# Optimization experiments

Measured on AMD Instinct MI355X. Metric: run time of the kernel, lower is better.

The kernel has to match this reference:

```python
import jax, jax.numpy as jnp
import numpy as np

BN_EPS = 1e-5
NUM_GRAPHS = 64

def _bn(h, gamma, beta):
    # BatchNorm1d over node dim, training-mode (batch statistics, biased var)
    mu = jnp.mean(h, axis=0)
    var = jnp.mean(jnp.square(h - mu), axis=0)
    return gamma * (h - mu) * jax.lax.rsqrt(var + BN_EPS) + beta

def _gin_conv(x, src, dst, Wa, ba, gamma, beta, Wb, bb):
    # sum-aggregate neighbor features: agg[v] = sum_{(u,v) in E} x[u]
    n = x.shape[0]
    agg = jax.ops.segment_sum(x[src], dst, num_segments=n)
    h = x + agg  # eps = 0 (default GINConv)
    h = jax.nn.relu(_bn(h @ Wa + ba, gamma, beta))
    return jax.nn.relu(h @ Wb + bb)

def setup_inputs() -> dict:
    key = jax.random.key(0)
    ks = jax.random.split(key, 16)
    N, E, IN, D, OUT = 50000, 800000, 128, 512, 10
    x = jax.random.normal(ks[0], (N, IN), dtype=jnp.float32)
    edge_index = jax.random.randint(ks[1], (2, E), 0, N, dtype=jnp.int64)
    batch = jnp.sort(jax.random.randint(ks[2], (N,), 0, NUM_GRAPHS, dtype=jnp.int64))
    def lin(k, i, o):
        return jax.random.normal(k, (i, o), dtype=jnp.float32) / np.sqrt(i)
    return {
        "x": x, "edge_index": edge_index, "batch": batch,
        "W1a": lin(ks[3], IN, D), "b1a": jnp.zeros((D,), jnp.float32),
        "g1": jnp.ones((D,), jnp.float32), "be1": jnp.zeros((D,), jnp.float32),
        "W1b": lin(ks[4], D, D), "b1b": jnp.zeros((D,), jnp.float32),
        "W2a": lin(ks[5], D, D), "b2a": jnp.zeros((D,), jnp.float32),
        "g2": jnp.ones((D,), jnp.float32), "be2": jnp.zeros((D,), jnp.float32),
        "W2b": lin(ks[6], D, D), "b2b": jnp.zeros((D,), jnp.float32),
        "Wl1": lin(ks[7], D, D), "bl1": jnp.zeros((D,), jnp.float32),
        "Wl2": lin(ks[8], D, OUT), "bl2": jnp.zeros((OUT,), jnp.float32),
    }

def reference(x, edge_index, batch, W1a, b1a, g1, be1, W1b, b1b,
              W2a, b2a, g2, be2, W2b, b2b, Wl1, bl1, Wl2, bl2):
    src, dst = edge_index[0], edge_index[1]
    h = _gin_conv(x, src, dst, W1a, b1a, g1, be1, W1b, b1b)
    h = _gin_conv(h, src, dst, W2a, b2a, g2, be2, W2b, b2b)
    pooled = jax.ops.segment_sum(h, batch, num_segments=NUM_GRAPHS)  # [G, D]
    out = jax.nn.relu(pooled @ Wl1 + bl1)
    return out @ Wl2 + bl2  # [G, out_channels]
```

## Files before the change

kernel.cpp:

```cpp
#include <hip/hip_runtime.h>
#include <cstdint>
#include <cstddef>

#define N_NODES  50000
#define N_EDGES  800000
#define DIM_IN   128
#define DIM_H    512
#define N_GRAPHS 64
#define DIM_OUT  10
#define BN_EPS   1e-5f
#define SCAN_B   196

typedef _Float16 h16;
using f16x8 = __attribute__((ext_vector_type(8))) _Float16;
using f32x4 = __attribute__((ext_vector_type(4))) float;

__device__ inline float4 add4(float4 a, float4 b) {
    return make_float4(a.x + b.x, a.y + b.y, a.z + b.z, a.w + b.w);
}

__global__ __launch_bounds__(256) void k_wcast_all(
    const float* __restrict__ W1a, const float* __restrict__ W1b,
    const float* __restrict__ W2a, const float* __restrict__ W2b,
    h16* __restrict__ Wt1a, h16* __restrict__ Wt1b,
    h16* __restrict__ Wt2a, h16* __restrict__ Wt2b,
    int* __restrict__ deg, float* __restrict__ pooled)
{
    int gtid = blockIdx.x * 256 + threadIdx.x;
    for (int i = gtid; i < N_NODES; i += 416 * 256) deg[i] = 0;
    for (int i = gtid; i < N_GRAPHS * DIM_H; i += 416 * 256) pooled[i] = 0.f;

    int b = blockIdx.x;
    const float* W; h16* Wt; int K, base;
    if (b < 32)       { W = W1a; Wt = Wt1a; K = DIM_IN; base = 0; }
    else if (b < 160) { W = W1b; Wt = Wt1b; K = DIM_H;  base = 32; }
    else if (b < 288) { W = W2a; Wt = Wt2a; K = DIM_H;  base = 160; }
    else              { W = W2b; Wt = Wt2b; K = DIM_H;  base = 288; }
    int t = (b - base) * 256 + threadIdx.x;
    int total = (K >> 3) * DIM_H;
    if (t >= total) return;
    int k8 = t / DIM_H;
    int n  = t - k8 * DIM_H;
    f16x8 o;
#pragma unroll
    for (int j = 0; j < 8; ++j)
        o[j] = (h16)W[(size_t)(k8 * 8 + j) * DIM_H + n];
    *reinterpret_cast<f16x8*>(&Wt[(size_t)n * K + k8 * 8]) = o;
}

__global__ __launch_bounds__(256) void k_deg(
    const int* __restrict__ dst, int* __restrict__ deg)
{
    int t = blockIdx.x * 256 + threadIdx.x;
    if (t < N_EDGES) atomicAdd(&deg[dst[t]], 1);
}

__global__ __launch_bounds__(256) void k_scan1(
    const int* __restrict__ deg, int* __restrict__ bsum)
{
    __shared__ int s[256];
    int tid = threadIdx.x;
    int i = blockIdx.x * 256 + tid;
    s[tid] = (i < N_NODES) ? deg[i] : 0;
    __syncthreads();
    for (int off = 128; off > 0; off >>= 1) {
        if (tid < off) s[tid] += s[tid + off];
        __syncthreads();
    }
    if (tid == 0) bsum[blockIdx.x] = s[0];
}

__global__ __launch_bounds__(256) void k_scan2(
    const int* __restrict__ bsum, int* __restrict__ boff)
{
    __shared__ int s[256];
    int tid = threadIdx.x;
    s[tid] = (tid < SCAN_B) ? bsum[tid] : 0;
    __syncthreads();
    for (int off = 1; off < 256; off <<= 1) {
        int u = (tid >= off) ? s[tid - off] : 0;
        __syncthreads();
        s[tid] += u;
        __syncthreads();
    }
    if (tid < SCAN_B) boff[tid] = (tid == 0) ? 0 : s[tid - 1];
}

__global__ __launch_bounds__(256) void k_scan3(
    const int* __restrict__ deg, const int* __restrict__ boff,
    int* __restrict__ rowptr, int* __restrict__ cursor,
    float* __restrict__ csum)
{
    __shared__ int s[256];
    int tid = threadIdx.x;
    int i = blockIdx.x * 256 + tid;
    int v = (i < N_NODES) ? deg[i] : 0;
    s[tid] = v;
    __syncthreads();
    for (int off = 1; off < 256; off <<= 1) {
        int u = (tid >= off) ? s[tid - off] : 0;
        __syncthreads();
        s[tid] += u;
        __syncthreads();
    }
    int excl = s[tid] - v + boff[blockIdx.x];
    if (i < N_NODES) {
        rowptr[i] = excl;
        cursor[i] = excl;
        if (i == N_NODES - 1) rowptr[N_NODES] = excl + v;
    }
    if (blockIdx.x == 0)
        for (int z = tid; z < 2 * DIM_H; z += 256) csum[z] = 0.f;
}

__global__ __launch_bounds__(256) void k_fill(
    const int* __restrict__ src, const int* __restrict__ dst,
    int* __restrict__ cursor, int* __restrict__ eidx)
{
    int t = blockIdx.x * 256 + threadIdx.x;
    if (t >= N_EDGES) return;
    int pos = atomicAdd(&cursor[dst[t]], 1);
    eidx[pos] = src[t];
}

__global__ __launch_bounds__(256) void k_gather128(
    const float4* __restrict__ X, const int* __restrict__ rowptr,
    const int* __restrict__ eidx, f16x8* __restrict__ out)
{
    int t = blockIdx.x * 256 + threadIdx.x;
    int v = t >> 4, lane = t & 15;
    if (v >= N_NODES) return;
    int r0 = rowptr[v], r1 = rowptr[v + 1];
    float4 a0 = X[(size_t)v * 32 + lane * 2];
    float4 a1 = X[(size_t)v * 32 + lane * 2 + 1];
    for (int j = r0; j < r1; ++j) {
        int s = eidx[j];
        a0 = add4(a0, X[(size_t)s * 32 + lane * 2]);
        a1 = add4(a1, X[(size_t)s * 32 + lane * 2 + 1]);
    }
    f16x8 o;
    o[0] = (h16)a0.x; o[1] = (h16)a0.y; o[2] = (h16)a0.z; o[3] = (h16)a0.w;
    o[4] = (h16)a1.x; o[5] = (h16)a1.y; o[6] = (h16)a1.z; o[7] = (h16)a1.w;
    out[(size_t)v * 16 + lane] = o;
}

__global__ __launch_bounds__(256) void k_gather512h(
    const f16x8* __restrict__ X, const int* __restrict__ rowptr,
    const int* __restrict__ eidx, f16x8* __restrict__ out,
    float* __restrict__ csum)
{
    if (blockIdx.x == 0)
        for (int z = threadIdx.x; z < 2 * DIM_H; z += 256) csum[z] = 0.f;

    int t = blockIdx.x * 256 + threadIdx.x;
    int v = t >> 6, lane = t & 63;
    if (v >= N_NODES) return;
    int r0 = rowptr[v], r1 = rowptr[v + 1];
    f16x8 sv = X[(size_t)v * 64 + lane];
    float a[8];
#pragma unroll
    for (int i = 0; i < 8; ++i) a[i] = (float)sv[i];
    int j = r0;
    for (; j + 7 < r1; j += 8) {
        f16x8 b0 = X[(size_t)eidx[j]     * 64 + lane];
        f16x8 b1 = X[(size_t)eidx[j + 1] * 64 + lane];
        f16x8 b2 = X[(size_t)eidx[j + 2] * 64 + lane];
        f16x8 b3 = X[(size_t)eidx[j + 3] * 64 + lane];
        f16x8 b4 = X[(size_t)eidx[j + 4] * 64 + lane];
        f16x8 b5 = X[(size_t)eidx[j + 5] * 64 + lane];
        f16x8 b6 = X[(size_t)eidx[j + 6] * 64 + lane];
        f16x8 b7 = X[(size_t)eidx[j + 7] * 64 + lane];
#pragma unroll
        for (int i = 0; i < 8; ++i)
            a[i] += (((float)b0[i] + (float)b1[i]) + ((float)b2[i] + (float)b3[i]))
                  + (((float)b4[i] + (float)b5[i]) + ((float)b6[i] + (float)b7[i]));
    }
    for (; j + 1 < r1; j += 2) {
        f16x8 b0 = X[(size_t)eidx[j]     * 64 + lane];
        f16x8 b1 = X[(size_t)eidx[j + 1] * 64 + lane];
#pragma unroll
        for (int i = 0; i < 8; ++i) a[i] += (float)b0[i] + (float)b1[i];
    }
    if (j < r1) {
        f16x8 b = X[(size_t)eidx[j] * 64 + lane];
#pragma unroll
        for (int i = 0; i < 8; ++i) a[i] += (float)b[i];
    }
    f16x8 o;
#pragma unroll
    for (int i = 0; i < 8; ++i) o[i] = (h16)a[i];
    out[(size_t)v * 64 + lane] = o;
}

template<bool AFFINE, bool RELU, bool STATS>
__global__ __launch_bounds__(512) void k_gemm_mfma(
    const h16* __restrict__ A, const h16* __restrict__ Bt,
    const float* __restrict__ bias,
    float* __restrict__ csum, float* __restrict__ csq,
    const float* __restrict__ gam, const float* __restrict__ bet,
    h16* __restrict__ C, int M, int N, int K, int lda)
{
    __shared__ f16x8 As[128 * 4];
    __shared__ f16x8 Bs[256 * 4];
    __shared__ float sfl[DIM_H], cfl[DIM_H];

    const int tid  = threadIdx.x;
    const int lane = tid & 63;
    const int w    = tid >> 6;
    const int wr   = w >> 2;
    const int wc   = w & 3;
    const int l15  = lane & 15;
    const int lk   = lane >> 4;
    const int m0   = blockIdx.x * 128;
    const int n0   = blockIdx.y * 256;

    if (AFFINE) {
        const float invM = 1.0f / (float)N_NODES;
        for (int cc = tid; cc < K; cc += 512) {
            float mu  = csum[cc] * invM;
            float var = csq[cc] * invM - mu * mu;
            float s   = gam[cc] * rsqrtf(var + BN_EPS);
            sfl[cc] = s;
            cfl[cc] = bet[cc] - mu * s;
        }
        __syncthreads();
    }

    const int a_row = tid >> 2;
    const int kb    = tid & 3;
    const int aswz  = kb ^ (a_row & 3);
    int ar = m0 + a_row; if (ar >= M) ar = M - 1;
    const h16* aptr = A + (size_t)ar * lda + kb * 8;
    const int b_col = tid >> 2;
    const int bswz  = kb ^ (b_col & 3);
    const h16* bptr = Bt + (size_t)(n0 + b_col) * K + kb * 8;
    const size_t bstride = (size_t)128 * K;

    f32x4 acc[4][4];
#pragma unroll
    for (int m = 0; m < 4; ++m)
#pragma unroll
        for (int n = 0; n < 4; ++n)
            acc[m][n] = (f32x4){0.f, 0.f, 0.f, 0.f};

    f16x8 av, bw0, bw1;

    auto load_tile = [&](int k0) {
        av  = *reinterpret_cast<const f16x8*>(aptr + k0);
        if (AFFINE) {
            int kk = k0 + kb * 8;
            float4 s0 = *reinterpret_cast<const float4*>(&sfl[kk]);
            float4 s1 = *reinterpret_cast<const float4*>(&sfl[kk + 4]);
            float4 c0 = *reinterpret_cast<const float4*>(&cfl[kk]);
            float4 c1 = *reinterpret_cast<const float4*>(&cfl[kk + 4]);
            float sarr[8] = {s0.x, s0.y, s0.z, s0.w, s1.x, s1.y, s1.z, s1.w};
            float carr[8] = {c0.x, c0.y, c0.z, c0.w, c1.x, c1.y, c1.z, c1.w};
#pragma unroll
            for (int i = 0; i < 8; ++i)
                av[i] = (h16)fmaxf(fmaf((float)av[i], sarr[i], carr[i]), 0.f);
        }
        bw0 = *reinterpret_cast<const f16x8*>(bptr + k0);
        bw1 = *reinterpret_cast<const f16x8*>(bptr + bstride + k0);
    };

    load_tile(0);

    for (int k0 = 0; k0 < K; k0 += 32) {
        __syncthreads();
        As[a_row * 4 + aswz]          = av;
        Bs[b_col * 4 + bswz]          = bw0;
        Bs[(b_col + 128) * 4 + bswz]  = bw1;
        __syncthreads();

        if (k0 + 32 < K) load_tile(k0 + 32);

        f16x8 af[4], bf[4];
#pragma unroll
        for (int m = 0; m < 4; ++m) {
            int row = wr * 64 + m * 16 + l15;
            af[m] = As[row * 4 + (lk ^ (row & 3))];
        }
#pragma unroll
        for (int n = 0; n < 4; ++n) {
            int col = wc * 64 + n * 16 + l15;
            bf[n] = Bs[col * 4 + (lk ^ (col & 3))];
        }
#pragma unroll
        for (int m = 0; m < 4; ++m)
#pragma unroll
            for (int n = 0; n < 4; ++n)
                acc[m][n] = __builtin_amdgcn_mfma_f32_16x16x32_f16(
                    af[m], bf[n], acc[m][n], 0, 0, 0);
    }

#pragma unroll
    for (int n = 0; n < 4; ++n) {
        int col = n0 + wc * 64 + n * 16 + l15;
        float bb = bias[col];
        float sp = 0.f, qp = 0.f;
#pragma unroll
        for (int m = 0; m < 4; ++m) {
            int row0 = m0 + wr * 64 + m * 16 + lk * 4;
#pragma unroll
            for (int r = 0; r < 4; ++r) {
                int row = row0 + r;
                if (row < M) {
                    float v = acc[m][n][r] + bb;
                    if (STATS) { sp += v; qp += v * v; }
                    if (RELU) v = fmaxf(v, 0.f);
                    C[(size_t)row * N + col] = (h16)v;
                }
            }
        }
        if (STATS) {
            sp += __shfl_xor(sp, 16); qp += __shfl_xor(qp, 16);
            sp += __shfl_xor(sp, 32); qp += __shfl_xor(qp, 32);
            if (lk == 0) {
                atomicAdd(&csum[col], sp);
                atomicAdd(&csq[col], qp);
            }
        }
    }
}

__global__ __launch_bounds__(256) void k_pool(
    const h16* __restrict__ H, const int* __restrict__ batch,
    float* __restrict__ pooled)
{
    __shared__ int bg[128];
    int base = blockIdx.x * 128;
    if (threadIdx.x < 128) {
        int r = base + threadIdx.x;
        bg[threadIdx.x] = (r < N_NODES) ? batch[r] : -1;
    }
    __syncthreads();
    int c0 = threadIdx.x;
    float a0 = 0.f, a1 = 0.f;
    int cur = bg[0];
    for (int r = 0; r < 128; ++r) {
        int g = bg[r];
        if (g < 0) break;
        if (g != cur) {
            atomicAdd(&pooled[cur * DIM_H + c0],       a0);
            atomicAdd(&pooled[cur * DIM_H + c0 + 256], a1);
            a0 = a1 = 0.f;
            cur = g;
        }
        size_t row = (size_t)(base + r);
        a0 += (float)H[row * DIM_H + c0];
        a1 += (float)H[row * DIM_H + c0 + 256];
    }
    if (cur >= 0) {
        atomicAdd(&pooled[cur * DIM_H + c0],       a0);
        atomicAdd(&pooled[cur * DIM_H + c0 + 256], a1);
    }
}

__global__ __launch_bounds__(512) void k_head(
    const float* __restrict__ pooled,
    const float* __restrict__ Wl1, const float* __restrict__ bl1,
    const float* __restrict__ Wl2, const float* __restrict__ bl2,
    float* __restrict__ out)
{
    __shared__ float rowp[DIM_H];
    __shared__ float qv[DIM_H];
    int g = blockIdx.x, c = threadIdx.x;
    rowp[c] = pooled[(size_t)g * DIM_H + c];
    __syncthreads();
    float acc = 0.f;
    for (int k = 0; k < DIM_H; ++k)
        acc = fmaf(rowp[k], Wl1[(size_t)k * DIM_H + c], acc);
    qv[c] = fmaxf(acc + bl1[c], 0.f);
    __syncthreads();
    if (c < DIM_OUT) {
        float a2 = 0.f;
        for (int k = 0; k < DIM_H; ++k)
            a2 = fmaf(qv[k], Wl2[(size_t)k * DIM_OUT + c], a2);
        out[g * DIM_OUT + c] = a2 + bl2[c];
    }
}

extern "C" void kernel_launch(void* const* d_in, const int* in_sizes, int n_in,
                              void* d_out, int out_size, void* d_ws, size_t ws_size,
                              hipStream_t stream)
{
    const float* x   = (const float*)d_in[0];
    const int*   ei  = (const int*)d_in[1];
    const int*   src = ei;
    const int*   dst = ei + N_EDGES;
    const int*   batch = (const int*)d_in[2];
    const float* W1a = (const float*)d_in[3];
    const float* b1a = (const float*)d_in[4];
    const float* g1  = (const float*)d_in[5];
    const float* be1 = (const float*)d_in[6];
    const float* W1b = (const float*)d_in[7];
    const float* b1b = (const float*)d_in[8];
    const float* W2a = (const float*)d_in[9];
    const float* b2a = (const float*)d_in[10];
    const float* g2  = (const float*)d_in[11];
    const float* be2 = (const float*)d_in[12];
    const float* W2b = (const float*)d_in[13];
    const float* b2b = (const float*)d_in[14];
    const float* Wl1 = (const float*)d_in[15];
    const float* bl1 = (const float*)d_in[16];
    const float* Wl2 = (const float*)d_in[17];
    const float* bl2 = (const float*)d_in[18];

    char* ws = (char*)d_ws;
    const size_t ROW_H = (size_t)N_NODES * DIM_H * 2;

    if (ws_size < 110000000ull) {
        hipMemsetAsync(d_out, 0, (size_t)out_size * 4, stream);
        return;
    }
    h16* B1h = (h16*)(ws + 0);
    h16* B2h = (h16*)(ws + ROW_H);
    h16* XAh = B2h;
    char* cp  = ws + 2 * ROW_H;
    int* deg    = (int*)(cp + 0);
    int* rowptr = (int*)(cp + 200192);
    int* cursor = (int*)(cp + 400384);
    int* eidx   = (int*)(cp + 600576);
    char* sm    = cp + 3800576;
    float* csum   = (float*)(sm + 0);
    float* csq    = (float*)(sm + 2048);
    float* pooled = (float*)(sm + 4096);
    char* wt = sm + 4096 + 131072;
    h16* Wt1a = (h16*)(wt);
    h16* Wt1b = (h16*)(wt + 131072);
    h16* Wt2a = (h16*)(wt + 131072 + 524288);
    h16* Wt2b = (h16*)(wt + 131072 + 2 * 524288);
    int* bsum = (int*)(wt + 131072 + 3 * 524288);
    int* boff = bsum + 256;

    const dim3 gemm_grid(391, 2);
    const int EB = (N_EDGES + 255) / 256;

    k_wcast_all<<<416, 256, 0, stream>>>(W1a, W1b, W2a, W2b,
                                         Wt1a, Wt1b, Wt2a, Wt2b, deg, pooled);
    k_deg<<<EB, 256, 0, stream>>>(dst, deg);
    k_scan1<<<SCAN_B, 256, 0, stream>>>(deg, bsum);
    k_scan2<<<1, 256, 0, stream>>>(bsum, boff);
    k_scan3<<<SCAN_B, 256, 0, stream>>>(deg, boff, rowptr, cursor, csum);
    k_fill<<<EB, 256, 0, stream>>>(src, dst, cursor, eidx);

    k_gather128<<<(N_NODES * 16 + 255) / 256, 256, 0, stream>>>(
        (const float4*)x, rowptr, eidx, (f16x8*)XAh);
    k_gemm_mfma<false, false, true><<<gemm_grid, 512, 0, stream>>>(
        XAh, Wt1a, b1a, csum, csq, nullptr, nullptr, B1h,
        N_NODES, DIM_H, DIM_IN, DIM_IN);
    k_gemm_mfma<true, true, false><<<gemm_grid, 512, 0, stream>>>(
        B1h, Wt1b, b1b, csum, csq, g1, be1, B2h,
        N_NODES, DIM_H, DIM_H, DIM_H);

    k_gather512h<<<(N_NODES * 64) / 256, 256, 0, stream>>>(
        (const f16x8*)B2h, rowptr, eidx, (f16x8*)B1h, csum);
    k_gemm_mfma<false, false, true><<<gemm_grid, 512, 0, stream>>>(
        B1h, Wt2a, b2a, csum, csq, nullptr, nullptr, B2h,
        N_NODES, DIM_H, DIM_H, DIM_H);
    k_gemm_mfma<true, true, false><<<gemm_grid, 512, 0, stream>>>(
        B2h, Wt2b, b2b, csum, csq, g2, be2, B1h,
        N_NODES, DIM_H, DIM_H, DIM_H);

    k_pool<<<(N_NODES + 127) / 128, 256, 0, stream>>>(B1h, batch, pooled);
    k_head<<<N_GRAPHS, 512, 0, stream>>>(pooled, Wl1, bl1, Wl2, bl2,
                                         (float*)d_out);
}
```

Before: 598.8 us.

## Widen GEMM tile to full 512 columns, fuse scan kernels, nontemporal gather stores

The MFMA GEMM now computes all 512 output columns per block (8 column fragments per wave, 4 B loads per thread), halving the grid and reading each A tile once instead of twice. The middle scan kernel is folded into the final scan, so every block re-scans the block sums itself and one launch is removed. Gather outputs are written with nontemporal stores. The wider tile doubles accumulator registers and LDS, which risks lower occupancy and spills, and the 391-block grid may underfill the device.

```diff
diff --git a/kernel.cpp b/kernel.cpp
--- a/kernel.cpp
+++ b/kernel.cpp
@@ -70,11 +70,14 @@
     if (tid == 0) bsum[blockIdx.x] = s[0];
 }
 
-__global__ __launch_bounds__(256) void k_scan2(
-    const int* __restrict__ bsum, int* __restrict__ boff)
+__global__ __launch_bounds__(256) void k_scan3(
+    const int* __restrict__ deg, const int* __restrict__ bsum,
+    int* __restrict__ rowptr, int* __restrict__ cursor,
+    float* __restrict__ csum)
 {
     __shared__ int s[256];
     int tid = threadIdx.x;
+
     s[tid] = (tid < SCAN_B) ? bsum[tid] : 0;
     __syncthreads();
     for (int off = 1; off < 256; off <<= 1) {
@@ -83,16 +86,9 @@
         s[tid] += u;
         __syncthreads();
     }
-    if (tid < SCAN_B) boff[tid] = (tid == 0) ? 0 : s[tid - 1];
-}
-
-__global__ __launch_bounds__(256) void k_scan3(
-    const int* __restrict__ deg, const int* __restrict__ boff,
-    int* __restrict__ rowptr, int* __restrict__ cursor,
-    float* __restrict__ csum)
-{
-    __shared__ int s[256];
-    int tid = threadIdx.x;
+    int bo = (blockIdx.x == 0) ? 0 : s[blockIdx.x - 1];
+    __syncthreads();
+
     int i = blockIdx.x * 256 + tid;
     int v = (i < N_NODES) ? deg[i] : 0;
     s[tid] = v;
@@ -103,7 +99,7 @@
         s[tid] += u;
         __syncthreads();
     }
-    int excl = s[tid] - v + boff[blockIdx.x];
+    int excl = s[tid] - v + bo;
     if (i < N_NODES) {
         rowptr[i] = excl;
         cursor[i] = excl;
@@ -141,7 +137,7 @@
     f16x8 o;
     o[0] = (h16)a0.x; o[1] = (h16)a0.y; o[2] = (h16)a0.z; o[3] = (h16)a0.w;
     o[4] = (h16)a1.x; o[5] = (h16)a1.y; o[6] = (h16)a1.z; o[7] = (h16)a1.w;
-    out[(size_t)v * 16 + lane] = o;
+    __builtin_nontemporal_store(o, &out[(size_t)v * 16 + lane]);
 }
 
 __global__ __launch_bounds__(256) void k_gather512h(
@@ -189,7 +185,7 @@
     f16x8 o;
 #pragma unroll
     for (int i = 0; i < 8; ++i) o[i] = (h16)a[i];
-    out[(size_t)v * 64 + lane] = o;
+    __builtin_nontemporal_store(o, &out[(size_t)v * 64 + lane]);
 }
 
 template<bool AFFINE, bool RELU, bool STATS>
@@ -201,7 +197,7 @@
     h16* __restrict__ C, int M, int N, int K, int lda)
 {
     __shared__ f16x8 As[128 * 4];
-    __shared__ f16x8 Bs[256 * 4];
+    __shared__ f16x8 Bs[512 * 4];
     __shared__ float sfl[DIM_H], cfl[DIM_H];
 
     const int tid  = threadIdx.x;
@@ -212,7 +208,6 @@
     const int l15  = lane & 15;
     const int lk   = lane >> 4;
     const int m0   = blockIdx.x * 128;
-    const int n0   = blockIdx.y * 256;
 
     if (AFFINE) {
         const float invM = 1.0f / (float)N_NODES;
@@ -233,17 +228,17 @@
     const h16* aptr = A + (size_t)ar * lda + kb * 8;
     const int b_col = tid >> 2;
     const int bswz  = kb ^ (b_col & 3);
-    const h16* bptr = Bt + (size_t)(n0 + b_col) * K + kb * 8;
+    const h16* bptr = Bt + (size_t)b_col * K + kb * 8;
     const size_t bstride = (size_t)128 * K;
 
-    f32x4 acc[4][4];
+    f32x4 acc[4][8];
 #pragma unroll
     for (int m = 0; m < 4; ++m)
 #pragma unroll
-        for (int n = 0; n < 4; ++n)
+        for (int n = 0; n < 8; ++n)
             acc[m][n] = (f32x4){0.f, 0.f, 0.f, 0.f};
 
-    f16x8 av, bw0, bw1;
+    f16x8 av, bw0, bw1, bw2, bw3;
 
     auto load_tile = [&](int k0) {
         av  = *reinterpret_cast<const f16x8*>(aptr + k0);
@@ -261,6 +256,8 @@
         }
         bw0 = *reinterpret_cast<const f16x8*>(bptr + k0);
         bw1 = *reinterpret_cast<const f16x8*>(bptr + bstride + k0);
+        bw2 = *reinterpret_cast<const f16x8*>(bptr + 2 * bstride + k0);
+        bw3 = *reinterpret_cast<const f16x8*>(bptr + 3 * bstride + k0);
     };
 
     load_tile(0);
@@ -270,32 +267,34 @@
         As[a_row * 4 + aswz]          = av;
         Bs[b_col * 4 + bswz]          = bw0;
         Bs[(b_col + 128) * 4 + bswz]  = bw1;
+        Bs[(b_col + 256) * 4 + bswz]  = bw2;
+        Bs[(b_col + 384) * 4 + bswz]  = bw3;
         __syncthreads();
 
         if (k0 + 32 < K) load_tile(k0 + 32);
 
-        f16x8 af[4], bf[4];
+        f16x8 af[4], bf[8];
 #pragma unroll
         for (int m = 0; m < 4; ++m) {
             int row = wr * 64 + m * 16 + l15;
             af[m] = As[row * 4 + (lk ^ (row & 3))];
         }
 #pragma unroll
-        for (int n = 0; n < 4; ++n) {
-            int col = wc * 64 + n * 16 + l15;
+        for (int n = 0; n < 8; ++n) {
+            int col = wc * 128 + n * 16 + l15;
             bf[n] = Bs[col * 4 + (lk ^ (col & 3))];
         }
 #pragma unroll
         for (int m = 0; m < 4; ++m)
 #pragma unroll
-            for (int n = 0; n < 4; ++n)
+            for (int n = 0; n < 8; ++n)
                 acc[m][n] = __builtin_amdgcn_mfma_f32_16x16x32_f16(
                     af[m], bf[n], acc[m][n], 0, 0, 0);
     }
 
 #pragma unroll
-    for (int n = 0; n < 4; ++n) {
-        int col = n0 + wc * 64 + n * 16 + l15;
+    for (int n = 0; n < 8; ++n) {
+        int col = wc * 128 + n * 16 + l15;
         float bb = bias[col];
         float sp = 0.f, qp = 0.f;
 #pragma unroll
@@ -431,17 +430,15 @@
     h16* Wt2a = (h16*)(wt + 131072 + 524288);
     h16* Wt2b = (h16*)(wt + 131072 + 2 * 524288);
     int* bsum = (int*)(wt + 131072 + 3 * 524288);
-    int* boff = bsum + 256;
-
-    const dim3 gemm_grid(391, 2);
+
+    const dim3 gemm_grid(391);
     const int EB = (N_EDGES + 255) / 256;
 
     k_wcast_all<<<416, 256, 0, stream>>>(W1a, W1b, W2a, W2b,
                                          Wt1a, Wt1b, Wt2a, Wt2b, deg, pooled);
     k_deg<<<EB, 256, 0, stream>>>(dst, deg);
     k_scan1<<<SCAN_B, 256, 0, stream>>>(deg, bsum);
-    k_scan2<<<1, 256, 0, stream>>>(bsum, boff);
-    k_scan3<<<SCAN_B, 256, 0, stream>>>(deg, boff, rowptr, cursor, csum);
+    k_scan3<<<SCAN_B, 256, 0, stream>>>(deg, bsum, rowptr, cursor, csum);
     k_fill<<<EB, 256, 0, stream>>>(src, dst, cursor, eidx);
 
     k_gather128<<<(N_NODES * 16 + 255) / 256, 256, 0, stream>>>(
```

Result: slower. 663.1 us (+10.7%).
